# Kernel tuning notes

Measured on AMD Instinct MI355X. Metric: run time of the kernel, lower is better.

The kernel has to match this reference:

```python
import jax, jax.numpy as jnp
import numpy as np

N_NODES = 50000
N_EDGES = 800000
N_GRAPHS = 64
F_IN = 128
HID = 64
HEADS = 4
N_CLS = 10
NEG_SLOPE = 0.2


def _glorot(key, shape):
    fan_in, fan_out = shape[-1], shape[-2] if len(shape) > 1 else shape[-1]
    lim = jnp.sqrt(6.0 / (fan_in + fan_out))
    return jax.random.uniform(key, shape, jnp.float32, -lim, lim)


def setup_inputs() -> dict:
    key = jax.random.key(0)
    ks = jax.random.split(key, 20)
    x = jax.random.normal(ks[0], (N_NODES, F_IN), jnp.float32)
    edge_index = jax.random.randint(ks[1], (2, N_EDGES), 0, N_NODES, jnp.int32)
    batch = jnp.sort(jax.random.randint(ks[2], (N_NODES,), 0, N_GRAPHS, jnp.int32))
    HC = HID * HEADS
    return {
        "x": x, "edge_index": edge_index, "batch": batch,
        # node embedding Linear(F_IN -> HID)
        "W_emb": _glorot(ks[3], (HID, F_IN)), "b_emb": jnp.zeros((HID,), jnp.float32),
        # gat1: HID -> HID, heads=4, concat
        "W1": _glorot(ks[4], (HC, HID)),
        "a_src1": _glorot(ks[5], (HEADS, HID)), "a_dst1": _glorot(ks[6], (HEADS, HID)),
        "b1": jnp.zeros((HC,), jnp.float32),
        # gat2: HC -> HID, heads=4, concat
        "W2": _glorot(ks[7], (HC, HC)),
        "a_src2": _glorot(ks[8], (HEADS, HID)), "a_dst2": _glorot(ks[9], (HEADS, HID)),
        "b2": jnp.zeros((HC,), jnp.float32),
        # gat3: HC -> HID, heads=1, mean
        "W3": _glorot(ks[10], (HID, HC)),
        "a_src3": _glorot(ks[11], (1, HID)), "a_dst3": _glorot(ks[12], (1, HID)),
        "b3": jnp.zeros((HID,), jnp.float32),
        # classifier: Linear(2*HID -> HID), ReLU, Linear(HID -> N_CLS)
        "Wc1": _glorot(ks[13], (HID, 2 * HID)), "bc1": jnp.zeros((HID,), jnp.float32),
        "Wc2": _glorot(ks[14], (N_CLS, HID)), "bc2": jnp.zeros((N_CLS,), jnp.float32),
    }


def _gat_layer(x, src, dst, W, a_src, a_dst, b, concat):
    """PyG-style GATConv (eval mode, self-loops already in src/dst)."""
    N = x.shape[0]
    H, C = a_src.shape
    h = (x @ W.T).reshape(N, H, C)                       # [N,H,C]
    s = jnp.einsum("nhc,hc->nh", h, a_src)               # [N,H]
    d = jnp.einsum("nhc,hc->nh", h, a_dst)               # [N,H]
    e = jax.nn.leaky_relu(s[src] + d[dst], NEG_SLOPE)    # [E,H]
    emax = jax.lax.stop_gradient(jax.ops.segment_max(e, dst, num_segments=N))
    emax = jnp.where(jnp.isfinite(emax), emax, 0.0)
    ex = jnp.exp(e - emax[dst])
    den = jax.ops.segment_sum(ex, dst, num_segments=N)   # [N,H]
    alpha = ex / (den[dst] + 1e-16)                      # segment softmax
    out = jax.ops.segment_sum(h[src] * alpha[:, :, None], dst, num_segments=N)
    out = out.reshape(N, H * C) if concat else out.mean(axis=1)
    return out + b


def reference(x, edge_index, batch, W_emb, b_emb, W1, a_src1, a_dst1, b1,
              W2, a_src2, a_dst2, b2, W3, a_src3, a_dst3, b3, Wc1, bc1, Wc2, bc2):
    N = x.shape[0]
    loops = jnp.arange(N, dtype=edge_index.dtype)
    src = jnp.concatenate([edge_index[0], loops])
    dst = jnp.concatenate([edge_index[1], loops])

    h = x @ W_emb.T + b_emb
    h = jax.nn.elu(_gat_layer(h, src, dst, W1, a_src1, a_dst1, b1, True))
    h = jax.nn.elu(_gat_layer(h, src, dst, W2, a_src2, a_dst2, b2, True))
    h = jax.nn.elu(_gat_layer(h, src, dst, W3, a_src3, a_dst3, b3, False))

    counts = jax.ops.segment_sum(jnp.ones((N,), h.dtype), batch, num_segments=N_GRAPHS)
    mean = jax.ops.segment_sum(h, batch, num_segments=N_GRAPHS) / jnp.maximum(counts, 1.0)[:, None]
    mx = jax.ops.segment_max(h, batch, num_segments=N_GRAPHS)
    mx = jnp.where(counts[:, None] > 0, mx, 0.0)
    g = jnp.concatenate([mean, mx], axis=1)              # [B, 2*HID]

    g = jax.nn.relu(g @ Wc1.T + bc1)
    return g @ Wc2.T + bc2                               # [B, N_CLS]
```

## Files before the change

### kernel.cpp

```cpp
#include <hip/hip_runtime.h>
#include <math.h>

#define NG 64
#define F_IN 128
#define NEG_SLOPE 0.2f

typedef __attribute__((ext_vector_type(8))) short s16x8;
typedef __attribute__((ext_vector_type(4))) float f32x4;

static __device__ __forceinline__ float elu_f(float x) { return x > 0.f ? x : expm1f(x); }
static __device__ __forceinline__ float lrelu(float x) { return x > 0.f ? x : NEG_SLOPE * x; }
static __device__ __forceinline__ unsigned enc_f32(float x) {
    unsigned u = __float_as_uint(x);
    return (u & 0x80000000u) ? ~u : (u | 0x80000000u);
}
static __device__ __forceinline__ float dec_f32(unsigned u) {
    unsigned b = (u & 0x80000000u) ? (u & 0x7fffffffu) : ~u;
    return __uint_as_float(b);
}
static __device__ __forceinline__ unsigned short bf16_rn(float x) {
    unsigned u = __float_as_uint(x);
    unsigned r = u + 0x7FFFu + ((u >> 16) & 1u);
    return (unsigned short)(r >> 16);
}
static __device__ __forceinline__ float bf16_to_f32(unsigned short h) {
    return __uint_as_float(((unsigned)h) << 16);
}

static __device__ __forceinline__ size_t fragaddr(int row, int k, int K) {
    return ((size_t)(row >> 4) * (K >> 5) + (k >> 5)) * 512
         + (size_t)(((k & 31) >> 3) * 128 + (row & 15) * 8 + (k & 7));
}

__global__ void convert_frag(const float* __restrict__ in, unsigned short* __restrict__ hi,
                             unsigned short* __restrict__ lo, int R, int K) {
    int t = blockIdx.x * blockDim.x + threadIdx.x;
    if (t * 8 >= R * K) return;
    int row = (t * 8) / K;
    int k0 = (t * 8) % K;
    float4 v0 = *(const float4*)&in[(size_t)row * K + k0];
    float4 v1 = *(const float4*)&in[(size_t)row * K + k0 + 4];
    float v[8] = {v0.x, v0.y, v0.z, v0.w, v1.x, v1.y, v1.z, v1.w};
    unsigned short h[8], l[8];
    #pragma unroll
    for (int i = 0; i < 8; ++i) {
        h[i] = bf16_rn(v[i]);
        l[i] = bf16_rn(v[i] - bf16_to_f32(h[i]));
    }
    size_t a = fragaddr(row, k0, K);
    *(ushort4*)&hi[a]     = make_ushort4(h[0], h[1], h[2], h[3]);
    *(ushort4*)&hi[a + 4] = make_ushort4(h[4], h[5], h[6], h[7]);
    *(ushort4*)&lo[a]     = make_ushort4(l[0], l[1], l[2], l[3]);
    *(ushort4*)&lo[a + 4] = make_ushort4(l[4], l[5], l[6], l[7]);
}

__global__ void uvec_kernel(const float* __restrict__ W1, const float* __restrict__ a1s,
                            const float* __restrict__ a1d,
                            float* __restrict__ us, float* __restrict__ ud) {
    int h = threadIdx.x >> 6;
    int i = threadIdx.x & 63;
    float s = 0.f, d = 0.f;
    for (int o = 0; o < 64; ++o) {
        float w = W1[(h * 64 + o) * 64 + i];
        s = fmaf(w, a1s[h * 64 + o], s);
        d = fmaf(w, a1d[h * 64 + o], d);
    }
    us[h * 64 + i] = s;
    ud[h * 64 + i] = d;
}

__global__ void hist_kernel(const int* __restrict__ ei, int* __restrict__ cnt, int E, int N) {
    int e = blockIdx.x * blockDim.x + threadIdx.x;
    int ET = E + N;
    if (e >= ET) return;
    int dst = (e < E) ? ei[E + e] : (e - E);
    atomicAdd(&cnt[dst], 1);
}

__global__ void scan1_kernel(const int* __restrict__ cnt, int* __restrict__ excl,
                             int* __restrict__ bsum, int n) {
    __shared__ int sm[256];
    int t = threadIdx.x;
    int base = blockIdx.x * 1024 + t * 4;
    int v[4];
    #pragma unroll
    for (int u = 0; u < 4; ++u) { int idx = base + u; v[u] = (idx < n) ? cnt[idx] : 0; }
    int tsum = v[0] + v[1] + v[2] + v[3];
    sm[t] = tsum;
    __syncthreads();
    for (int off = 1; off < 256; off <<= 1) {
        int y = (t >= off) ? sm[t - off] : 0;
        __syncthreads();
        sm[t] += y;
        __syncthreads();
    }
    int run = sm[t] - tsum;
    #pragma unroll
    for (int u = 0; u < 4; ++u) {
        int idx = base + u;
        if (idx < n) excl[idx] = run;
        run += v[u];
    }
    if (t == 255) bsum[blockIdx.x] = sm[255];
}

__global__ void scan2_kernel(int* __restrict__ bsum, int* __restrict__ offs, int nb, int n) {
    if (blockIdx.x == 0 && threadIdx.x == 0) {
        int run = 0;
        for (int b = 0; b < nb; ++b) { int t = bsum[b]; bsum[b] = run; run += t; }
        offs[n] = run;
    }
}

__global__ void scan3_kernel(int* __restrict__ offs, const int* __restrict__ bsum, int n) {
    int base = blockIdx.x * 1024 + threadIdx.x * 4;
    int add = bsum[blockIdx.x];
    #pragma unroll
    for (int u = 0; u < 4; ++u) { int idx = base + u; if (idx < n) offs[idx] += add; }
}

__global__ void scatter_kernel(const int* __restrict__ ei, const int* __restrict__ offs,
                               int* __restrict__ cursor, int* __restrict__ csr_src, int E, int N) {
    int e = blockIdx.x * blockDim.x + threadIdx.x;
    int ET = E + N;
    if (e >= ET) return;
    int src, dst;
    if (e < E) { src = ei[e]; dst = ei[E + e]; }
    else       { src = e - E; dst = e - E; }
    int pos = offs[dst] + atomicAdd(&cursor[dst], 1);
    csr_src[pos] = src;
}

template<int K, int AK, int BN, int HATT, bool SHARED, bool SLICED, bool DO_ELU, int OUTM>
__global__ __launch_bounds__(256) void gemm_frag(const unsigned short* __restrict__ Ahi,
                                                 const unsigned short* __restrict__ Alo,
                                                 const unsigned short* __restrict__ Whi,
                                                 const unsigned short* __restrict__ Wlo,
                                                 void* __restrict__ OutV,
                                                 unsigned short* __restrict__ Ohi,
                                                 unsigned short* __restrict__ Olo,
                                                 int M,
                                                 const float* __restrict__ bias,
                                                 const float* __restrict__ asrc,
                                                 const float* __restrict__ adst,
                                                 float* __restrict__ S, float* __restrict__ D,
                                                 int N) {
    constexpr int RF = (BN == 256) ? 4 : 2;
    const int t = threadIdx.x;
    const int lane = t & 63;
    const int w = t >> 6;
    const int lj = lane & 15;
    const int kg = lane >> 4;
    const int n0 = blockIdx.x * ((BN == 256) ? 64 : 128);
    const int m0 = blockIdx.y * BN;
    const int rbase = (BN == 256) ? 0 : w * 32;
    const int cbase = (BN == 256) ? w * 64 : 0;
    const int aoff = SLICED ? blockIdx.y * K : 0;
    const unsigned short* __restrict__ WhiB = SLICED ? Whi + (size_t)blockIdx.y * BN * K : Whi;
    const unsigned short* __restrict__ WloB = SLICED ? Wlo + (size_t)blockIdx.y * BN * K : Wlo;

    f32x4 acc[RF][4];
    #pragma unroll
    for (int rf = 0; rf < RF; ++rf)
        #pragma unroll
        for (int cf = 0; cf < 4; ++cf) acc[rf][cf] = (f32x4){0.f, 0.f, 0.f, 0.f};

    for (int kc = 0; kc < K; kc += 32) {
        s16x8 ah[RF], al[RF];
        #pragma unroll
        for (int rf = 0; rf < RF; ++rf) {
            size_t a = fragaddr(n0 + rbase + rf * 16 + lj, aoff + kc + kg * 8, AK);
            ah[rf] = *(const s16x8*)&Ahi[a];
            al[rf] = *(const s16x8*)&Alo[a];
        }
        #pragma unroll
        for (int cf = 0; cf < 4; ++cf) {
            int bcol = (SLICED ? 0 : m0) + cbase + cf * 16 + lj;
            size_t b = fragaddr(bcol, kc + kg * 8, K);
            s16x8 bh = *(const s16x8*)&WhiB[b];
            s16x8 bl = *(const s16x8*)&WloB[b];
            #pragma unroll
            for (int rf = 0; rf < RF; ++rf) {
                acc[rf][cf] = __builtin_amdgcn_mfma_f32_16x16x32_bf16(ah[rf], bh, acc[rf][cf], 0, 0, 0);
                acc[rf][cf] = __builtin_amdgcn_mfma_f32_16x16x32_bf16(ah[rf], bl, acc[rf][cf], 0, 0, 0);
                acc[rf][cf] = __builtin_amdgcn_mfma_f32_16x16x32_bf16(al[rf], bh, acc[rf][cf], 0, 0, 0);
            }
        }
    }

    #pragma unroll
    for (int cf = 0; cf < 4; ++cf) {
        int gcol = m0 + cbase + cf * 16 + lj;
        float bv = bias ? bias[gcol] : 0.f;
        #pragma unroll
        for (int rf = 0; rf < RF; ++rf) {
            #pragma unroll
            for (int r = 0; r < 4; ++r) {
                int gn = n0 + rbase + rf * 16 + (lane >> 4) * 4 + r;
                if (gn < N) {
                    float o = acc[rf][cf][r] + bv;
                    if (DO_ELU) o = elu_f(o);
                    if (OUTM == 0) {
                        ((float*)OutV)[(size_t)gn * M + gcol] = o;
                    } else if (OUTM == 1) {
                        ((unsigned short*)OutV)[(size_t)gn * M + gcol] = bf16_rn(o);
                    } else {
                        unsigned short hv = bf16_rn(o);
                        unsigned short lv = bf16_rn(o - bf16_to_f32(hv));
                        size_t a2 = fragaddr(gn, gcol, M);
                        Ohi[a2] = hv; Olo[a2] = lv;
                    }
                }
            }
        }
    }
    if (HATT > 0) {
        const int HS = SHARED ? HATT : 1;
        #pragma unroll
        for (int hh = 0; hh < HS; ++hh) {
            const int head = SHARED ? hh : w;
            float aw[4], dw[4], bw[4];
            #pragma unroll
            for (int c2 = 0; c2 < 4; ++c2) {
                aw[c2] = asrc[head * 64 + c2 * 16 + lj];
                dw[c2] = adst[head * 64 + c2 * 16 + lj];
                bw[c2] = bias ? bias[m0 + cbase + c2 * 16 + lj] : 0.f;
            }
            #pragma unroll
            for (int rf = 0; rf < RF; ++rf) {
                #pragma unroll
                for (int r = 0; r < 4; ++r) {
                    float sp = 0.f, dp = 0.f;
                    #pragma unroll
                    for (int c2 = 0; c2 < 4; ++c2) {
                        float vv = acc[rf][c2][r] + bw[c2];
                        sp = fmaf(vv, aw[c2], sp);
                        dp = fmaf(vv, dw[c2], dp);
                    }
                    #pragma unroll
                    for (int off = 1; off < 16; off <<= 1) {
                        sp += __shfl_xor(sp, off);
                        dp += __shfl_xor(dp, off);
                    }
                    if (lj == 0) {
                        int gn = n0 + rbase + rf * 16 + (lane >> 4) * 4 + r;
                        if (gn < N) { S[gn * HATT + head] = sp; D[gn * HATT + head] = dp; }
                    }
                }
            }
        }
    }
}

__global__ __launch_bounds__(256, 8) void gat_agg_x(const float* __restrict__ xA,
                                                    const float* __restrict__ s,
                                                    const float* __restrict__ d,
                                                    const int* __restrict__ offs,
                                                    const int* __restrict__ csr_src,
                                                    unsigned short* __restrict__ Gh,
                                                    unsigned short* __restrict__ Gl,
                                                    int N) {
    __shared__ float stash[4][64 * 5];
    int wv = threadIdx.x >> 6;
    int lane = threadIdx.x & 63;
    int node = (blockIdx.x * blockDim.x + threadIdx.x) >> 6;
    if (node >= N) return;
    float* st = stash[wv];
    int e0 = offs[node], e1 = offs[node + 1];
    float4 dv4 = *(const float4*)&d[node * 4];
    float dd[4] = {dv4.x, dv4.y, dv4.z, dv4.w};
    float mrun[4] = {-INFINITY, -INFINITY, -INFINITY, -INFINITY};
    float den[4] = {0.f, 0.f, 0.f, 0.f};
    float acc[4] = {0.f, 0.f, 0.f, 0.f};

    for (int base = e0; base < e1; base += 64) {
        int cnt = min(64, e1 - base);
        float ev[4] = {-INFINITY, -INFINITY, -INFINITY, -INFINITY};
        if (lane < cnt) {
            int src = csr_src[base + lane];
            float4 sv = *(const float4*)&s[src * 4];
            ev[0] = lrelu(sv.x + dd[0]); ev[1] = lrelu(sv.y + dd[1]);
            ev[2] = lrelu(sv.z + dd[2]); ev[3] = lrelu(sv.w + dd[3]);
            st[lane * 5 + 0] = ev[0]; st[lane * 5 + 1] = ev[1];
            st[lane * 5 + 2] = ev[2]; st[lane * 5 + 3] = ev[3];
            st[lane * 5 + 4] = __int_as_float(src);
        }
        #pragma unroll
        for (int h = 0; h < 4; ++h) {
            float m = ev[h];
            #pragma unroll
            for (int off = 32; off; off >>= 1) m = fmaxf(m, __shfl_xor(m, off));
            float mnew = fmaxf(mrun[h], m);
            float scale = __expf(mrun[h] - mnew);
            acc[h] *= scale; den[h] *= scale;
            mrun[h] = mnew;
        }
        int k = 0;
        for (; k + 4 <= cnt; k += 4) {
            int si[4];
            #pragma unroll
            for (int u = 0; u < 4; ++u) si[u] = __float_as_int(st[(k + u) * 5 + 4]);
            float vx[4];
            #pragma unroll
            for (int u = 0; u < 4; ++u) vx[u] = xA[(size_t)si[u] * 64 + lane];
            #pragma unroll
            for (int u = 0; u < 4; ++u) {
                #pragma unroll
                for (int h = 0; h < 4; ++h) {
                    float p = __expf(st[(k + u) * 5 + h] - mrun[h]);
                    den[h] += p;
                    acc[h] = fmaf(p, vx[u], acc[h]);
                }
            }
        }
        for (; k < cnt; ++k) {
            int src = __float_as_int(st[k * 5 + 4]);
            float v = xA[(size_t)src * 64 + lane];
            #pragma unroll
            for (int h = 0; h < 4; ++h) {
                float p = __expf(st[k * 5 + h] - mrun[h]);
                den[h] += p;
                acc[h] = fmaf(p, v, acc[h]);
            }
        }
    }
    #pragma unroll
    for (int h = 0; h < 4; ++h) {
        float v = acc[h] / (den[h] + 1e-16f);
        unsigned short hv = bf16_rn(v);
        unsigned short lv = bf16_rn(v - bf16_to_f32(hv));
        size_t a = fragaddr(node, h * 64 + lane, 256);
        Gh[a] = hv; Gl[a] = lv;
    }
}

template<int H, bool FRAGOUT>
__global__ __launch_bounds__(256, 8) void gat_agg(const unsigned short* __restrict__ hp,
                                                  const float* __restrict__ s,
                                                  const float* __restrict__ d,
                                                  const int* __restrict__ offs,
                                                  const int* __restrict__ csr_src,
                                                  const float* __restrict__ bias,
                                                  float* __restrict__ outF,
                                                  unsigned short* __restrict__ outHi,
                                                  unsigned short* __restrict__ outLo,
                                                  int N) {
    const int SW = (H == 4) ? 5 : 2;
    __shared__ float stash[4][64 * 5];
    int wv = threadIdx.x >> 6;
    int lane = threadIdx.x & 63;
    int node = (blockIdx.x * blockDim.x + threadIdx.x) >> 6;
    if (node >= N) return;
    float* st = stash[wv];
    int e0 = offs[node], e1 = offs[node + 1];

    float dd[H];
    #pragma unroll
    for (int h = 0; h < H; ++h) dd[h] = d[node * H + h];

    const int hd = (H == 4) ? (lane >> 4) : 0;

    float mrun = -INFINITY;
    float acc0 = 0.f, acc1 = 0.f, acc2 = 0.f, acc3 = 0.f, den = 0.f;

    for (int base = e0; base < e1; base += 64) {
        int cnt = min(64, e1 - base);
        float ev[H];
        #pragma unroll
        for (int h = 0; h < H; ++h) ev[h] = -INFINITY;
        if (lane < cnt) {
            int src = csr_src[base + lane];
            if (H == 4) {
                float4 sv = *(const float4*)&s[src * 4];
                ev[0] = lrelu(sv.x + dd[0]); ev[1] = lrelu(sv.y + dd[1]);
                ev[2] = lrelu(sv.z + dd[2]); ev[3] = lrelu(sv.w + dd[3]);
                st[lane * 5 + 0] = ev[0]; st[lane * 5 + 1] = ev[1];
                st[lane * 5 + 2] = ev[2]; st[lane * 5 + 3] = ev[3];
                st[lane * 5 + 4] = __int_as_float(src);
            } else {
                ev[0] = lrelu(s[src] + dd[0]);
                st[lane * 2 + 0] = ev[0];
                st[lane * 2 + 1] = __int_as_float(src);
            }
        }
        float mc[H];
        #pragma unroll
        for (int h = 0; h < H; ++h) {
            float m = ev[h];
            #pragma unroll
            for (int off = 32; off; off >>= 1) m = fmaxf(m, __shfl_xor(m, off));
            mc[h] = m;
        }
        float mch = mc[0];
        if (H == 4)
            mch = (lane & 32) ? ((lane & 16) ? mc[3] : mc[2]) : ((lane & 16) ? mc[1] : mc[0]);
        float mnew = fmaxf(mrun, mch);
        float scale = __expf(mrun - mnew);
        acc0 *= scale; acc1 *= scale; acc2 *= scale; acc3 *= scale; den *= scale;
        mrun = mnew;

        int k = 0;
        for (; k + 4 <= cnt; k += 4) {
            float ea = st[(k + 0) * SW + hd];
            float eb = st[(k + 1) * SW + hd];
            float ec = st[(k + 2) * SW + hd];
            float ed = st[(k + 3) * SW + hd];
            int sa = __float_as_int(st[(k + 0) * SW + SW - 1]);
            int sb = __float_as_int(st[(k + 1) * SW + SW - 1]);
            int sc = __float_as_int(st[(k + 2) * SW + SW - 1]);
            int sd_ = __float_as_int(st[(k + 3) * SW + SW - 1]);
            float pa = __expf(ea - mrun);
            float pb = __expf(eb - mrun);
            float pc = __expf(ec - mrun);
            float pd = __expf(ed - mrun);
            den += (pa + pb) + (pc + pd);
            if (H == 4) {
                uint2 ua = *(const uint2*)&hp[(size_t)sa * 256 + lane * 4];
                uint2 ub = *(const uint2*)&hp[(size_t)sb * 256 + lane * 4];
                uint2 uc = *(const uint2*)&hp[(size_t)sc * 256 + lane * 4];
                uint2 ud = *(const uint2*)&hp[(size_t)sd_ * 256 + lane * 4];
                acc0 = fmaf(pa, __uint_as_float((ua.x & 0xffffu) << 16), acc0);
                acc1 = fmaf(pa, __uint_as_float(ua.x & 0xffff0000u), acc1);
                acc2 = fmaf(pa, __uint_as_float((ua.y & 0xffffu) << 16), acc2);
                acc3 = fmaf(pa, __uint_as_float(ua.y & 0xffff0000u), acc3);
                acc0 = fmaf(pb, __uint_as_float((ub.x & 0xffffu) << 16), acc0);
                acc1 = fmaf(pb, __uint_as_float(ub.x & 0xffff0000u), acc1);
                acc2 = fmaf(pb, __uint_as_float((ub.y & 0xffffu) << 16), acc2);
                acc3 = fmaf(pb, __uint_as_float(ub.y & 0xffff0000u), acc3);
                acc0 = fmaf(pc, __uint_as_float((uc.x & 0xffffu) << 16), acc0);
                acc1 = fmaf(pc, __uint_as_float(uc.x & 0xffff0000u), acc1);
                acc2 = fmaf(pc, __uint_as_float((uc.y & 0xffffu) << 16), acc2);
                acc3 = fmaf(pc, __uint_as_float(uc.y & 0xffff0000u), acc3);
                acc0 = fmaf(pd, __uint_as_float((ud.x & 0xffffu) << 16), acc0);
                acc1 = fmaf(pd, __uint_as_float(ud.x & 0xffff0000u), acc1);
                acc2 = fmaf(pd, __uint_as_float((ud.y & 0xffffu) << 16), acc2);
                acc3 = fmaf(pd, __uint_as_float(ud.y & 0xffff0000u), acc3);
            } else {
                float ha = bf16_to_f32(hp[(size_t)sa * 64 + lane]);
                float hb = bf16_to_f32(hp[(size_t)sb * 64 + lane]);
                float hc = bf16_to_f32(hp[(size_t)sc * 64 + lane]);
                float hdv = bf16_to_f32(hp[(size_t)sd_ * 64 + lane]);
                acc0 = fmaf(pa, ha, acc0);
                acc0 = fmaf(pb, hb, acc0);
                acc0 = fmaf(pc, hc, acc0);
                acc0 = fmaf(pd, hdv, acc0);
            }
        }
        for (; k < cnt; ++k) {
            float e = st[k * SW + hd];
            int src = __float_as_int(st[k * SW + SW - 1]);
            float p = __expf(e - mrun);
            den += p;
            if (H == 4) {
                uint2 uv = *(const uint2*)&hp[(size_t)src * 256 + lane * 4];
                acc0 = fmaf(p, __uint_as_float((uv.x & 0xffffu) << 16), acc0);
                acc1 = fmaf(p, __uint_as_float(uv.x & 0xffff0000u), acc1);
                acc2 = fmaf(p, __uint_as_float((uv.y & 0xffffu) << 16), acc2);
                acc3 = fmaf(p, __uint_as_float(uv.y & 0xffff0000u), acc3);
            } else {
                acc0 = fmaf(p, bf16_to_f32(hp[(size_t)src * 64 + lane]), acc0);
            }
        }
    }

    float inv = 1.0f / (den + 1e-16f);
    if (H == 4) {
        float4 bv = *(const float4*)&bias[lane * 4];
        float o0 = elu_f(acc0 * inv + bv.x);
        float o1 = elu_f(acc1 * inv + bv.y);
        float o2 = elu_f(acc2 * inv + bv.z);
        float o3 = elu_f(acc3 * inv + bv.w);
        if (FRAGOUT) {
            unsigned short h0 = bf16_rn(o0), h1 = bf16_rn(o1), h2 = bf16_rn(o2), h3 = bf16_rn(o3);
            ushort4 hq = make_ushort4(h0, h1, h2, h3);
            ushort4 lq = make_ushort4(bf16_rn(o0 - bf16_to_f32(h0)),
                                      bf16_rn(o1 - bf16_to_f32(h1)),
                                      bf16_rn(o2 - bf16_to_f32(h2)),
                                      bf16_rn(o3 - bf16_to_f32(h3)));
            size_t a = fragaddr(node, lane * 4, 256);
            *(ushort4*)&outHi[a] = hq;
            *(ushort4*)&outLo[a] = lq;
        } else {
            float4 o = make_float4(o0, o1, o2, o3);
            *(float4*)&outF[(size_t)node * 256 + lane * 4] = o;
        }
    } else {
        outF[(size_t)node * 64 + lane] = elu_f(acc0 * inv + bias[lane]);
    }
}

__global__ void pool_init(float* gsum, unsigned* gmax, int* gcnt) {
    int t = blockIdx.x * blockDim.x + threadIdx.x;
    if (t < NG * 64) { gsum[t] = 0.f; gmax[t] = enc_f32(-INFINITY); }
    if (t < NG) gcnt[t] = 0;
}

__global__ void pool_reduce(const float* __restrict__ h3, const int* __restrict__ batch,
                            float* __restrict__ gsum, unsigned* __restrict__ gmax,
                            int* __restrict__ gcnt, int N, int per) {
    int w = (blockIdx.x * blockDim.x + threadIdx.x) >> 6;
    int lane = threadIdx.x & 63;
    int n0 = w * per;
    int n1 = min(N, n0 + per);
    float lsum = 0.f, lmax = -INFINITY;
    int cur = -1, cnt = 0;
    for (int n = n0; n < n1; ++n) {
        int g = batch[n];
        if (g != cur) {
            if (cur >= 0) {
                atomicAdd(&gsum[cur * 64 + lane], lsum);
                atomicMax(&gmax[cur * 64 + lane], enc_f32(lmax));
                if (lane == 0) atomicAdd(&gcnt[cur], cnt);
            }
            cur = g; lsum = 0.f; lmax = -INFINITY; cnt = 0;
        }
        float v = h3[(size_t)n * 64 + lane];
        lsum += v; lmax = fmaxf(lmax, v); cnt++;
    }
    if (cur >= 0) {
        atomicAdd(&gsum[cur * 64 + lane], lsum);
        atomicMax(&gmax[cur * 64 + lane], enc_f32(lmax));
        if (lane == 0) atomicAdd(&gcnt[cur], cnt);
    }
}

__global__ __launch_bounds__(128) void classifier(const float* __restrict__ gsum,
                                                  const unsigned* __restrict__ gmax,
                                                  const int* __restrict__ gcnt,
                                                  const float* __restrict__ Wc1,
                                                  const float* __restrict__ bc1,
                                                  const float* __restrict__ Wc2,
                                                  const float* __restrict__ bc2,
                                                  float* __restrict__ out) {
    __shared__ float gv[128];
    __shared__ float z1[64];
    int g = blockIdx.x, t = threadIdx.x;
    int cnt = gcnt[g];
    if (t < 64) {
        gv[t] = gsum[g * 64 + t] / fmaxf((float)cnt, 1.f);
    } else {
        float mx = dec_f32(gmax[g * 64 + (t - 64)]);
        gv[t] = (cnt > 0) ? mx : 0.f;
    }
    __syncthreads();
    if (t < 64) {
        float a = bc1[t];
        for (int k = 0; k < 128; ++k) a = fmaf(Wc1[t * 128 + k], gv[k], a);
        z1[t] = a > 0.f ? a : 0.f;
    }
    __syncthreads();
    if (t < 10) {
        float a = bc2[t];
        for (int k = 0; k < 64; ++k) a = fmaf(Wc2[t * 64 + k], z1[k], a);
        out[g * 10 + t] = a;
    }
}

extern "C" void kernel_launch(void* const* d_in, const int* in_sizes, int n_in,
                              void* d_out, int out_size, void* d_ws, size_t ws_size,
                              hipStream_t stream) {
    const float* x      = (const float*)d_in[0];
    const int*   ei     = (const int*)d_in[1];
    const int*   batch  = (const int*)d_in[2];
    const float* W_emb  = (const float*)d_in[3];
    const float* b_emb  = (const float*)d_in[4];
    const float* W1     = (const float*)d_in[5];
    const float* as1    = (const float*)d_in[6];
    const float* ad1    = (const float*)d_in[7];
    const float* b1     = (const float*)d_in[8];
    const float* W2     = (const float*)d_in[9];
    const float* as2    = (const float*)d_in[10];
    const float* ad2    = (const float*)d_in[11];
    const float* b2     = (const float*)d_in[12];
    const float* W3     = (const float*)d_in[13];
    const float* as3    = (const float*)d_in[14];
    const float* ad3    = (const float*)d_in[15];
    const float* b3     = (const float*)d_in[16];
    const float* Wc1    = (const float*)d_in[17];
    const float* bc1    = (const float*)d_in[18];
    const float* Wc2    = (const float*)d_in[19];
    const float* bc2    = (const float*)d_in[20];

    const int N = in_sizes[0] / F_IN;
    const int E = in_sizes[1] / 2;
    const int ET = E + N;
    const int GB64 = (N + 63) / 64;
    const int GB128 = (N + 127) / 128;
    const int ROWS_FR = ((N + 255) / 256) * 256;
    const size_t FR128 = (size_t)(ROWS_FR / 16) * (128 / 32) * 512;
    const size_t FR256 = (size_t)(ROWS_FR / 16) * (256 / 32) * 512;

    size_t off = 0;
    auto alloc = [&](size_t bytes) -> void* {
        void* p = (char*)d_ws + off;
        off += (bytes + 255) & ~(size_t)255;
        return p;
    };
    unsigned short* Xh  = (unsigned short*)alloc(FR128 * 2);
    unsigned short* Xl  = (unsigned short*)alloc(FR128 * 2);
    float*          Aemb= (float*)alloc((size_t)N * 64 * 4);
    unsigned short* Gh  = (unsigned short*)alloc(FR256 * 2);
    unsigned short* Gl  = (unsigned short*)alloc(FR256 * 2);
    unsigned short* C1h = (unsigned short*)alloc(FR256 * 2);
    unsigned short* C1l = (unsigned short*)alloc(FR256 * 2);
    unsigned short* H2b = (unsigned short*)alloc((size_t)N * 256 * 2);
    unsigned short* WhE = (unsigned short*)alloc(64 * 128 * 2);
    unsigned short* WlE = (unsigned short*)alloc(64 * 128 * 2);
    unsigned short* Wh1 = (unsigned short*)alloc(256 * 64 * 2);
    unsigned short* Wl1 = (unsigned short*)alloc(256 * 64 * 2);
    unsigned short* Wh2 = (unsigned short*)alloc(256 * 256 * 2);
    unsigned short* Wl2 = (unsigned short*)alloc(256 * 256 * 2);
    unsigned short* Wh3 = (unsigned short*)alloc(64 * 256 * 2);
    unsigned short* Wl3 = (unsigned short*)alloc(64 * 256 * 2);
    float*    us1     = (float*)alloc(4 * 64 * 4);
    float*    ud1     = (float*)alloc(4 * 64 * 4);
    float*    S       = (float*)alloc((size_t)N * 4 * 4);
    float*    D       = (float*)alloc((size_t)N * 4 * 4);
    int*      offs    = (int*)alloc((size_t)(N + 1) * 4);
    int*      cnt     = (int*)alloc((size_t)N * 4);
    int*      bsum    = (int*)alloc(64 * 4);
    int*      csr_src = (int*)alloc((size_t)ET * 4);
    float*    gsum    = (float*)alloc(NG * 64 * 4);
    unsigned* gmax    = (unsigned*)alloc(NG * 64 * 4);
    int*      gcnt    = (int*)alloc(NG * 4);
    (void)ws_size; (void)n_in; (void)out_size;

    const int SCB = (N + 1023) / 1024;

    convert_frag<<<(N * 128 / 8 + 255) / 256, 256, 0, stream>>>(x, Xh, Xl, N, 128);
    convert_frag<<<4, 256, 0, stream>>>(W_emb, WhE, WlE, 64, 128);
    convert_frag<<<8, 256, 0, stream>>>(W1, Wh1, Wl1, 256, 64);
    convert_frag<<<32, 256, 0, stream>>>(W2, Wh2, Wl2, 256, 256);
    convert_frag<<<8, 256, 0, stream>>>(W3, Wh3, Wl3, 64, 256);
    uvec_kernel<<<1, 256, 0, stream>>>(W1, as1, ad1, us1, ud1);

    hipMemsetAsync(cnt, 0, (size_t)N * 4, stream);
    hist_kernel<<<(ET + 255) / 256, 256, 0, stream>>>(ei, cnt, E, N);
    scan1_kernel<<<SCB, 256, 0, stream>>>(cnt, offs, bsum, N);
    scan2_kernel<<<1, 64, 0, stream>>>(bsum, offs, SCB, N);
    scan3_kernel<<<SCB, 256, 0, stream>>>(offs, bsum, N);
    hipMemsetAsync(cnt, 0, (size_t)N * 4, stream);
    scatter_kernel<<<(ET + 255) / 256, 256, 0, stream>>>(ei, offs, cnt, csr_src, E, N);

    const int NWV = (N * 64 + 255) / 256;

    gemm_frag<128, 128, 64, 4, true, false, false, 0><<<dim3(GB128, 1), 256, 0, stream>>>(
        Xh, Xl, WhE, WlE, Aemb, nullptr, nullptr, 64, b_emb, us1, ud1, S, D, N);
    gat_agg_x<<<NWV, 256, 0, stream>>>(Aemb, S, D, offs, csr_src, Gh, Gl, N);
    gemm_frag<64, 256, 64, 0, false, true, true, 3><<<dim3(GB128, 4), 256, 0, stream>>>(
        Gh, Gl, Wh1, Wl1, nullptr, C1h, C1l, 256, b1, nullptr, nullptr, nullptr, nullptr, N);
    gemm_frag<256, 256, 256, 4, false, false, false, 1><<<dim3(GB64, 1), 256, 0, stream>>>(
        C1h, C1l, Wh2, Wl2, H2b, nullptr, nullptr, 256, nullptr, as2, ad2, S, D, N);
    gat_agg<4, true><<<NWV, 256, 0, stream>>>(H2b, S, D, offs, csr_src, b2,
                                              nullptr, Gh, Gl, N);
    gemm_frag<256, 256, 64, 1, true, false, false, 1><<<dim3(GB128, 1), 256, 0, stream>>>(
        Gh, Gl, Wh3, Wl3, (unsigned short*)Aemb, nullptr, nullptr, 64, nullptr, as3, ad3, S, D, N);
    gat_agg<1, false><<<NWV, 256, 0, stream>>>((const unsigned short*)Aemb, S, D, offs, csr_src,
                                               b3, (float*)H2b, nullptr, nullptr, N);

    pool_init<<<16, 256, 0, stream>>>(gsum, gmax, gcnt);
    const int PBLK = 512;
    int per = (N + PBLK * 4 - 1) / (PBLK * 4);
    pool_reduce<<<PBLK, 256, 0, stream>>>((const float*)H2b, batch, gsum, gmax, gcnt, N, per);
    classifier<<<NG, 128, 0, stream>>>(gsum, gmax, gcnt, Wc1, bc1, Wc2, bc2, (float*)d_out);
}
```

Baseline: 539.1 us.

## Store embedding as bf16, split layer-2 aggregation across two waves, fuse setup kernels

The embedding GEMM now writes bf16 instead of fp32, which halves the gather traffic in the first attention aggregation. The 4-head aggregation is split so each node gets two wavefronts, each covering two heads. This doubles parallelism and shortens the per-node serial edge loop, at the cost of reading the edge list twice. The four weight-conversion launches become one kernel, and the scatter cursor is initialised from the scan, which removes a memset and an offset load. The bf16 embedding adds rounding error to layer-1 inputs.

```diff
diff --git a/kernel.cpp b/kernel.cpp
--- a/kernel.cpp
+++ b/kernel.cpp
@@ -30,6 +30,21 @@
 static __device__ __forceinline__ size_t fragaddr(int row, int k, int K) {
     return ((size_t)(row >> 4) * (K >> 5) + (k >> 5)) * 512
          + (size_t)(((k & 31) >> 3) * 128 + (row & 15) * 8 + (k & 7));
+}
+
+static __device__ __forceinline__ void frag_store8(const float* v, unsigned short* hi,
+                                                   unsigned short* lo, int row, int k0, int K) {
+    unsigned short h[8], l[8];
+    #pragma unroll
+    for (int i = 0; i < 8; ++i) {
+        h[i] = bf16_rn(v[i]);
+        l[i] = bf16_rn(v[i] - bf16_to_f32(h[i]));
+    }
+    size_t a = fragaddr(row, k0, K);
+    *(ushort4*)&hi[a]     = make_ushort4(h[0], h[1], h[2], h[3]);
+    *(ushort4*)&hi[a + 4] = make_ushort4(h[4], h[5], h[6], h[7]);
+    *(ushort4*)&lo[a]     = make_ushort4(l[0], l[1], l[2], l[3]);
+    *(ushort4*)&lo[a + 4] = make_ushort4(l[4], l[5], l[6], l[7]);
 }
 
 __global__ void convert_frag(const float* __restrict__ in, unsigned short* __restrict__ hi,
@@ -41,17 +56,29 @@
     float4 v0 = *(const float4*)&in[(size_t)row * K + k0];
     float4 v1 = *(const float4*)&in[(size_t)row * K + k0 + 4];
     float v[8] = {v0.x, v0.y, v0.z, v0.w, v1.x, v1.y, v1.z, v1.w};
-    unsigned short h[8], l[8];
-    #pragma unroll
-    for (int i = 0; i < 8; ++i) {
-        h[i] = bf16_rn(v[i]);
-        l[i] = bf16_rn(v[i] - bf16_to_f32(h[i]));
-    }
-    size_t a = fragaddr(row, k0, K);
-    *(ushort4*)&hi[a]     = make_ushort4(h[0], h[1], h[2], h[3]);
-    *(ushort4*)&hi[a + 4] = make_ushort4(h[4], h[5], h[6], h[7]);
-    *(ushort4*)&lo[a]     = make_ushort4(l[0], l[1], l[2], l[3]);
-    *(ushort4*)&lo[a + 4] = make_ushort4(l[4], l[5], l[6], l[7]);
+    frag_store8(v, hi, lo, row, k0, K);
+}
+
+__global__ void convert_weights(const float* __restrict__ We, const float* __restrict__ W1,
+                                const float* __restrict__ W2, const float* __restrict__ W3,
+                                unsigned short* WhE, unsigned short* WlE,
+                                unsigned short* Wh1, unsigned short* Wl1,
+                                unsigned short* Wh2, unsigned short* Wl2,
+                                unsigned short* Wh3, unsigned short* Wl3) {
+    int b = blockIdx.x;
+    const float* in; unsigned short* hi; unsigned short* lo; int R, K, base;
+    if (b < 4)       { in = We; hi = WhE; lo = WlE; R = 64;  K = 128; base = 0; }
+    else if (b < 12) { in = W1; hi = Wh1; lo = Wl1; R = 256; K = 64;  base = 4; }
+    else if (b < 44) { in = W2; hi = Wh2; lo = Wl2; R = 256; K = 256; base = 12; }
+    else             { in = W3; hi = Wh3; lo = Wl3; R = 64;  K = 256; base = 44; }
+    int t = (b - base) * 256 + threadIdx.x;
+    if (t * 8 >= R * K) return;
+    int row = (t * 8) / K;
+    int k0 = (t * 8) % K;
+    float4 v0 = *(const float4*)&in[(size_t)row * K + k0];
+    float4 v1 = *(const float4*)&in[(size_t)row * K + k0 + 4];
+    float v[8] = {v0.x, v0.y, v0.z, v0.w, v1.x, v1.y, v1.z, v1.w};
+    frag_store8(v, hi, lo, row, k0, K);
 }
 
 __global__ void uvec_kernel(const float* __restrict__ W1, const float* __restrict__ a1s,
@@ -112,22 +139,26 @@
     }
 }
 
-__global__ void scan3_kernel(int* __restrict__ offs, const int* __restrict__ bsum, int n) {
+__global__ void scan3_kernel(int* __restrict__ offs, const int* __restrict__ bsum,
+                             int* __restrict__ cur, int n) {
     int base = blockIdx.x * 1024 + threadIdx.x * 4;
     int add = bsum[blockIdx.x];
     #pragma unroll
-    for (int u = 0; u < 4; ++u) { int idx = base + u; if (idx < n) offs[idx] += add; }
-}
-
-__global__ void scatter_kernel(const int* __restrict__ ei, const int* __restrict__ offs,
-                               int* __restrict__ cursor, int* __restrict__ csr_src, int E, int N) {
+    for (int u = 0; u < 4; ++u) {
+        int idx = base + u;
+        if (idx < n) { int v = offs[idx] + add; offs[idx] = v; cur[idx] = v; }
+    }
+}
+
+__global__ void scatter_kernel(const int* __restrict__ ei, int* __restrict__ cur,
+                               int* __restrict__ csr_src, int E, int N) {
     int e = blockIdx.x * blockDim.x + threadIdx.x;
     int ET = E + N;
     if (e >= ET) return;
     int src, dst;
     if (e < E) { src = ei[e]; dst = ei[E + e]; }
     else       { src = e - E; dst = e - E; }
-    int pos = offs[dst] + atomicAdd(&cursor[dst], 1);
+    int pos = atomicAdd(&cur[dst], 1);
     csr_src[pos] = src;
 }
 
@@ -252,7 +283,7 @@
     }
 }
 
-__global__ __launch_bounds__(256, 8) void gat_agg_x(const float* __restrict__ xA,
+__global__ __launch_bounds__(256, 8) void gat_agg_x(const unsigned short* __restrict__ xb,
                                                     const float* __restrict__ s,
                                                     const float* __restrict__ d,
                                                     const int* __restrict__ offs,
@@ -302,7 +333,7 @@
             for (int u = 0; u < 4; ++u) si[u] = __float_as_int(st[(k + u) * 5 + 4]);
             float vx[4];
             #pragma unroll
-            for (int u = 0; u < 4; ++u) vx[u] = xA[(size_t)si[u] * 64 + lane];
+            for (int u = 0; u < 4; ++u) vx[u] = bf16_to_f32(xb[(size_t)si[u] * 64 + lane]);
             #pragma unroll
             for (int u = 0; u < 4; ++u) {
                 #pragma unroll
@@ -315,7 +346,7 @@
         }
         for (; k < cnt; ++k) {
             int src = __float_as_int(st[k * 5 + 4]);
-            float v = xA[(size_t)src * 64 + lane];
+            float v = bf16_to_f32(xb[(size_t)src * 64 + lane]);
             #pragma unroll
             for (int h = 0; h < 4; ++h) {
                 float p = __expf(st[k * 5 + h] - mrun[h]);
@@ -334,159 +365,185 @@
     }
 }
 
-template<int H, bool FRAGOUT>
-__global__ __launch_bounds__(256, 8) void gat_agg(const unsigned short* __restrict__ hp,
-                                                  const float* __restrict__ s,
-                                                  const float* __restrict__ d,
-                                                  const int* __restrict__ offs,
-                                                  const int* __restrict__ csr_src,
-                                                  const float* __restrict__ bias,
-                                                  float* __restrict__ outF,
-                                                  unsigned short* __restrict__ outHi,
-                                                  unsigned short* __restrict__ outLo,
-                                                  int N) {
-    const int SW = (H == 4) ? 5 : 2;
-    __shared__ float stash[4][64 * 5];
+template<bool FRAGOUT>
+__global__ __launch_bounds__(256, 8) void gat_agg2(const unsigned short* __restrict__ hp,
+                                                   const float* __restrict__ s,
+                                                   const float* __restrict__ d,
+                                                   const int* __restrict__ offs,
+                                                   const int* __restrict__ csr_src,
+                                                   const float* __restrict__ bias,
+                                                   float* __restrict__ outF,
+                                                   unsigned short* __restrict__ outHi,
+                                                   unsigned short* __restrict__ outLo,
+                                                   int N) {
+    __shared__ float stash[4][64 * 3];
+    int wv = threadIdx.x >> 6;
+    int lane = threadIdx.x & 63;
+    int gw = (blockIdx.x * blockDim.x + threadIdx.x) >> 6;
+    int node = gw >> 1;
+    int half = gw & 1;
+    if (node >= N) return;
+    float* st = stash[wv];
+    int e0 = offs[node], e1 = offs[node + 1];
+    const int h0 = half * 2;
+    float2 dv = *(const float2*)&d[node * 4 + h0];
+    const float dd0 = dv.x, dd1 = dv.y;
+    const int hh = lane >> 5;
+    const int ci = (lane & 31) * 2;
+    const int rowoff = (h0 + hh) * 64 + ci;
+
+    float mrun = -INFINITY;
+    float a0 = 0.f, a1 = 0.f, den = 0.f;
+
+    for (int base = e0; base < e1; base += 64) {
+        int cnt = min(64, e1 - base);
+        float ev0 = -INFINITY, ev1 = -INFINITY;
+        if (lane < cnt) {
+            int src = csr_src[base + lane];
+            float2 sv = *(const float2*)&s[src * 4 + h0];
+            ev0 = lrelu(sv.x + dd0);
+            ev1 = lrelu(sv.y + dd1);
+            st[lane * 3 + 0] = ev0;
+            st[lane * 3 + 1] = ev1;
+            st[lane * 3 + 2] = __int_as_float(src);
+        }
+        float m0 = ev0, m1 = ev1;
+        #pragma unroll
+        for (int off = 32; off; off >>= 1) {
+            m0 = fmaxf(m0, __shfl_xor(m0, off));
+            m1 = fmaxf(m1, __shfl_xor(m1, off));
+        }
+        float mch = hh ? m1 : m0;
+        float mnew = fmaxf(mrun, mch);
+        float scale = __expf(mrun - mnew);
+        a0 *= scale; a1 *= scale; den *= scale;
+        mrun = mnew;
+
+        int k = 0;
+        for (; k + 4 <= cnt; k += 4) {
+            float ea = st[(k + 0) * 3 + hh];
+            float eb = st[(k + 1) * 3 + hh];
+            float ec = st[(k + 2) * 3 + hh];
+            float ed = st[(k + 3) * 3 + hh];
+            int sa = __float_as_int(st[(k + 0) * 3 + 2]);
+            int sb = __float_as_int(st[(k + 1) * 3 + 2]);
+            int sc = __float_as_int(st[(k + 2) * 3 + 2]);
+            int sd_ = __float_as_int(st[(k + 3) * 3 + 2]);
+            float pa = __expf(ea - mrun);
+            float pb = __expf(eb - mrun);
+            float pc = __expf(ec - mrun);
+            float pd = __expf(ed - mrun);
+            den += (pa + pb) + (pc + pd);
+            unsigned ua = *(const unsigned*)&hp[(size_t)sa * 256 + rowoff];
+            unsigned ub = *(const unsigned*)&hp[(size_t)sb * 256 + rowoff];
+            unsigned uc = *(const unsigned*)&hp[(size_t)sc * 256 + rowoff];
+            unsigned ud = *(const unsigned*)&hp[(size_t)sd_ * 256 + rowoff];
+            a0 = fmaf(pa, __uint_as_float((ua & 0xffffu) << 16), a0);
+            a1 = fmaf(pa, __uint_as_float(ua & 0xffff0000u), a1);
+            a0 = fmaf(pb, __uint_as_float((ub & 0xffffu) << 16), a0);
+            a1 = fmaf(pb, __uint_as_float(ub & 0xffff0000u), a1);
+            a0 = fmaf(pc, __uint_as_float((uc & 0xffffu) << 16), a0);
+            a1 = fmaf(pc, __uint_as_float(uc & 0xffff0000u), a1);
+            a0 = fmaf(pd, __uint_as_float((ud & 0xffffu) << 16), a0);
+            a1 = fmaf(pd, __uint_as_float(ud & 0xffff0000u), a1);
+        }
+        for (; k < cnt; ++k) {
+            float e = st[k * 3 + hh];
+            int src = __float_as_int(st[k * 3 + 2]);
+            float p = __expf(e - mrun);
+            den += p;
+            unsigned uv = *(const unsigned*)&hp[(size_t)src * 256 + rowoff];
+            a0 = fmaf(p, __uint_as_float((uv & 0xffffu) << 16), a0);
+            a1 = fmaf(p, __uint_as_float(uv & 0xffff0000u), a1);
+        }
+    }
+
+    float inv = 1.0f / (den + 1e-16f);
+    float2 bv = *(const float2*)&bias[rowoff];
+    float o0 = elu_f(a0 * inv + bv.x);
+    float o1 = elu_f(a1 * inv + bv.y);
+    if (FRAGOUT) {
+        unsigned short hv0 = bf16_rn(o0), hv1 = bf16_rn(o1);
+        unsigned short lv0 = bf16_rn(o0 - bf16_to_f32(hv0));
+        unsigned short lv1 = bf16_rn(o1 - bf16_to_f32(hv1));
+        size_t a = fragaddr(node, rowoff, 256);
+        *(ushort2*)&outHi[a] = make_ushort2(hv0, hv1);
+        *(ushort2*)&outLo[a] = make_ushort2(lv0, lv1);
+    } else {
+        *(float2*)&outF[(size_t)node * 256 + rowoff] = make_float2(o0, o1);
+    }
+}
+
+__global__ __launch_bounds__(256, 8) void gat_agg1(const unsigned short* __restrict__ hp,
+                                                   const float* __restrict__ s,
+                                                   const float* __restrict__ d,
+                                                   const int* __restrict__ offs,
+                                                   const int* __restrict__ csr_src,
+                                                   const float* __restrict__ bias,
+                                                   float* __restrict__ outF, int N) {
+    __shared__ float stash[4][64 * 2];
     int wv = threadIdx.x >> 6;
     int lane = threadIdx.x & 63;
     int node = (blockIdx.x * blockDim.x + threadIdx.x) >> 6;
     if (node >= N) return;
     float* st = stash[wv];
     int e0 = offs[node], e1 = offs[node + 1];
-
-    float dd[H];
-    #pragma unroll
-    for (int h = 0; h < H; ++h) dd[h] = d[node * H + h];
-
-    const int hd = (H == 4) ? (lane >> 4) : 0;
+    float dd = d[node];
 
     float mrun = -INFINITY;
-    float acc0 = 0.f, acc1 = 0.f, acc2 = 0.f, acc3 = 0.f, den = 0.f;
+    float acc0 = 0.f, den = 0.f;
 
     for (int base = e0; base < e1; base += 64) {
         int cnt = min(64, e1 - base);
-        float ev[H];
-        #pragma unroll
-        for (int h = 0; h < H; ++h) ev[h] = -INFINITY;
+        float ev = -INFINITY;
         if (lane < cnt) {
             int src = csr_src[base + lane];
-            if (H == 4) {
-                float4 sv = *(const float4*)&s[src * 4];
-                ev[0] = lrelu(sv.x + dd[0]); ev[1] = lrelu(sv.y + dd[1]);
-                ev[2] = lrelu(sv.z + dd[2]); ev[3] = lrelu(sv.w + dd[3]);
-                st[lane * 5 + 0] = ev[0]; st[lane * 5 + 1] = ev[1];
-                st[lane * 5 + 2] = ev[2]; st[lane * 5 + 3] = ev[3];
-                st[lane * 5 + 4] = __int_as_float(src);
-            } else {
-                ev[0] = lrelu(s[src] + dd[0]);
-                st[lane * 2 + 0] = ev[0];
-                st[lane * 2 + 1] = __int_as_float(src);
-            }
-        }
-        float mc[H];
+            ev = lrelu(s[src] + dd);
+            st[lane * 2 + 0] = ev;
+            st[lane * 2 + 1] = __int_as_float(src);
+        }
+        float m = ev;
         #pragma unroll
-        for (int h = 0; h < H; ++h) {
-            float m = ev[h];
-            #pragma unroll
-            for (int off = 32; off; off >>= 1) m = fmaxf(m, __shfl_xor(m, off));
-            mc[h] = m;
-        }
-        float mch = mc[0];
-        if (H == 4)
-            mch = (lane & 32) ? ((lane & 16) ? mc[3] : mc[2]) : ((lane & 16) ? mc[1] : mc[0]);
-        float mnew = fmaxf(mrun, mch);
+        for (int off = 32; off; off >>= 1) m = fmaxf(m, __shfl_xor(m, off));
+        float mnew = fmaxf(mrun, m);
         float scale = __expf(mrun - mnew);
-        acc0 *= scale; acc1 *= scale; acc2 *= scale; acc3 *= scale; den *= scale;
+        acc0 *= scale; den *= scale;
         mrun = mnew;
 
         int k = 0;
         for (; k + 4 <= cnt; k += 4) {
-            float ea = st[(k + 0) * SW + hd];
-            float eb = st[(k + 1) * SW + hd];
-            float ec = st[(k + 2) * SW + hd];
-            float ed = st[(k + 3) * SW + hd];
-            int sa = __float_as_int(st[(k + 0) * SW + SW - 1]);
-            int sb = __float_as_int(st[(k + 1) * SW + SW - 1]);
-            int sc = __float_as_int(st[(k + 2) * SW + SW - 1]);
-            int sd_ = __float_as_int(st[(k + 3) * SW + SW - 1]);
+            float ea = st[(k + 0) * 2];
+            float eb = st[(k + 1) * 2];
+            float ec = st[(k + 2) * 2];
+            float ed = st[(k + 3) * 2];
+            int sa = __float_as_int(st[(k + 0) * 2 + 1]);
+            int sb = __float_as_int(st[(k + 1) * 2 + 1]);
+            int sc = __float_as_int(st[(k + 2) * 2 + 1]);
+            int sd_ = __float_as_int(st[(k + 3) * 2 + 1]);
             float pa = __expf(ea - mrun);
             float pb = __expf(eb - mrun);
             float pc = __expf(ec - mrun);
             float pd = __expf(ed - mrun);
             den += (pa + pb) + (pc + pd);
-            if (H == 4) {
-                uint2 ua = *(const uint2*)&hp[(size_t)sa * 256 + lane * 4];
-                uint2 ub = *(const uint2*)&hp[(size_t)sb * 256 + lane * 4];
-                uint2 uc = *(const uint2*)&hp[(size_t)sc * 256 + lane * 4];
-                uint2 ud = *(const uint2*)&hp[(size_t)sd_ * 256 + lane * 4];
-                acc0 = fmaf(pa, __uint_as_float((ua.x & 0xffffu) << 16), acc0);
-                acc1 = fmaf(pa, __uint_as_float(ua.x & 0xffff0000u), acc1);
-                acc2 = fmaf(pa, __uint_as_float((ua.y & 0xffffu) << 16), acc2);
-                acc3 = fmaf(pa, __uint_as_float(ua.y & 0xffff0000u), acc3);
-                acc0 = fmaf(pb, __uint_as_float((ub.x & 0xffffu) << 16), acc0);
-                acc1 = fmaf(pb, __uint_as_float(ub.x & 0xffff0000u), acc1);
-                acc2 = fmaf(pb, __uint_as_float((ub.y & 0xffffu) << 16), acc2);
-                acc3 = fmaf(pb, __uint_as_float(ub.y & 0xffff0000u), acc3);
-                acc0 = fmaf(pc, __uint_as_float((uc.x & 0xffffu) << 16), acc0);
-                acc1 = fmaf(pc, __uint_as_float(uc.x & 0xffff0000u), acc1);
-                acc2 = fmaf(pc, __uint_as_float((uc.y & 0xffffu) << 16), acc2);
-                acc3 = fmaf(pc, __uint_as_float(uc.y & 0xffff0000u), acc3);
-                acc0 = fmaf(pd, __uint_as_float((ud.x & 0xffffu) << 16), acc0);
-                acc1 = fmaf(pd, __uint_as_float(ud.x & 0xffff0000u), acc1);
-                acc2 = fmaf(pd, __uint_as_float((ud.y & 0xffffu) << 16), acc2);
-                acc3 = fmaf(pd, __uint_as_float(ud.y & 0xffff0000u), acc3);
-            } else {
-                float ha = bf16_to_f32(hp[(size_t)sa * 64 + lane]);
-                float hb = bf16_to_f32(hp[(size_t)sb * 64 + lane]);
-                float hc = bf16_to_f32(hp[(size_t)sc * 64 + lane]);
-                float hdv = bf16_to_f32(hp[(size_t)sd_ * 64 + lane]);
-                acc0 = fmaf(pa, ha, acc0);
-                acc0 = fmaf(pb, hb, acc0);
-                acc0 = fmaf(pc, hc, acc0);
-                acc0 = fmaf(pd, hdv, acc0);
-            }
+            float ha = bf16_to_f32(hp[(size_t)sa * 64 + lane]);
+            float hb = bf16_to_f32(hp[(size_t)sb * 64 + lane]);
+            float hc = bf16_to_f32(hp[(size_t)sc * 64 + lane]);
+            float hdv = bf16_to_f32(hp[(size_t)sd_ * 64 + lane]);
+            acc0 = fmaf(pa, ha, acc0);
+            acc0 = fmaf(pb, hb, acc0);
+            acc0 = fmaf(pc, hc, acc0);
+            acc0 = fmaf(pd, hdv, acc0);
         }
         for (; k < cnt; ++k) {
-            float e = st[k * SW + hd];
-            int src = __float_as_int(st[k * SW + SW - 1]);
+            float e = st[k * 2];
+            int src = __float_as_int(st[k * 2 + 1]);
             float p = __expf(e - mrun);
             den += p;
-            if (H == 4) {
-                uint2 uv = *(const uint2*)&hp[(size_t)src * 256 + lane * 4];
-                acc0 = fmaf(p, __uint_as_float((uv.x & 0xffffu) << 16), acc0);
-                acc1 = fmaf(p, __uint_as_float(uv.x & 0xffff0000u), acc1);
-                acc2 = fmaf(p, __uint_as_float((uv.y & 0xffffu) << 16), acc2);
-                acc3 = fmaf(p, __uint_as_float(uv.y & 0xffff0000u), acc3);
-            } else {
-                acc0 = fmaf(p, bf16_to_f32(hp[(size_t)src * 64 + lane]), acc0);
-            }
-        }
-    }
-
+            acc0 = fmaf(p, bf16_to_f32(hp[(size_t)src * 64 + lane]), acc0);
+        }
+    }
     float inv = 1.0f / (den + 1e-16f);
-    if (H == 4) {
-        float4 bv = *(const float4*)&bias[lane * 4];
-        float o0 = elu_f(acc0 * inv + bv.x);
-        float o1 = elu_f(acc1 * inv + bv.y);
-        float o2 = elu_f(acc2 * inv + bv.z);
-        float o3 = elu_f(acc3 * inv + bv.w);
-        if (FRAGOUT) {
-            unsigned short h0 = bf16_rn(o0), h1 = bf16_rn(o1), h2 = bf16_rn(o2), h3 = bf16_rn(o3);
-            ushort4 hq = make_ushort4(h0, h1, h2, h3);
-            ushort4 lq = make_ushort4(bf16_rn(o0 - bf16_to_f32(h0)),
-                                      bf16_rn(o1 - bf16_to_f32(h1)),
-                                      bf16_rn(o2 - bf16_to_f32(h2)),
-                                      bf16_rn(o3 - bf16_to_f32(h3)));
-            size_t a = fragaddr(node, lane * 4, 256);
-            *(ushort4*)&outHi[a] = hq;
-            *(ushort4*)&outLo[a] = lq;
-        } else {
-            float4 o = make_float4(o0, o1, o2, o3);
-            *(float4*)&outF[(size_t)node * 256 + lane * 4] = o;
-        }
-    } else {
-        outF[(size_t)node * 64 + lane] = elu_f(acc0 * inv + bias[lane]);
-    }
+    outF[(size_t)node * 64 + lane] = elu_f(acc0 * inv + bias[lane]);
 }
 
 __global__ void pool_init(float* gsum, unsigned* gmax, int* gcnt) {
@@ -598,7 +655,7 @@
     };
     unsigned short* Xh  = (unsigned short*)alloc(FR128 * 2);
     unsigned short* Xl  = (unsigned short*)alloc(FR128 * 2);
-    float*          Aemb= (float*)alloc((size_t)N * 64 * 4);
+    unsigned short* Aemb= (unsigned short*)alloc((size_t)N * 64 * 2);
     unsigned short* Gh  = (unsigned short*)alloc(FR256 * 2);
     unsigned short* Gl  = (unsigned short*)alloc(FR256 * 2);
     unsigned short* C1h = (unsigned short*)alloc(FR256 * 2);
@@ -628,35 +685,32 @@
     const int SCB = (N + 1023) / 1024;
 
     convert_frag<<<(N * 128 / 8 + 255) / 256, 256, 0, stream>>>(x, Xh, Xl, N, 128);
-    convert_frag<<<4, 256, 0, stream>>>(W_emb, WhE, WlE, 64, 128);
-    convert_frag<<<8, 256, 0, stream>>>(W1, Wh1, Wl1, 256, 64);
-    convert_frag<<<32, 256, 0, stream>>>(W2, Wh2, Wl2, 256, 256);
-    convert_frag<<<8, 256, 0, stream>>>(W3, Wh3, Wl3, 64, 256);
+    convert_weights<<<52, 256, 0, stream>>>(W_emb, W1, W2, W3, WhE, WlE, Wh1, Wl1,
+                                            Wh2, Wl2, Wh3, Wl3);
     uvec_kernel<<<1, 256, 0, stream>>>(W1, as1, ad1, us1, ud1);
 
     hipMemsetAsync(cnt, 0, (size_t)N * 4, stream);
     hist_kernel<<<(ET + 255) / 256, 256, 0, stream>>>(ei, cnt, E, N);
     scan1_kernel<<<SCB, 256, 0, stream>>>(cnt, offs, bsum, N);
     scan2_kernel<<<1, 64, 0, stream>>>(bsum, offs, SCB, N);
-    scan3_kernel<<<SCB, 256, 0, stream>>>(offs, bsum, N);
-    hipMemsetAsync(cnt, 0, (size_t)N * 4, stream);
-    scatter_kernel<<<(ET + 255) / 256, 256, 0, stream>>>(ei, offs, cnt, csr_src, E, N);
+    scan3_kernel<<<SCB, 256, 0, stream>>>(offs, bsum, cnt, N);
+    scatter_kernel<<<(ET + 255) / 256, 256, 0, stream>>>(ei, cnt, csr_src, E, N);
 
     const int NWV = (N * 64 + 255) / 256;
-
-    gemm_frag<128, 128, 64, 4, true, false, false, 0><<<dim3(GB128, 1), 256, 0, stream>>>(
+    const int NWV2 = (N * 128 + 255) / 256;
+
+    gemm_frag<128, 128, 64, 4, true, false, false, 1><<<dim3(GB128, 1), 256, 0, stream>>>(
         Xh, Xl, WhE, WlE, Aemb, nullptr, nullptr, 64, b_emb, us1, ud1, S, D, N);
     gat_agg_x<<<NWV, 256, 0, stream>>>(Aemb, S, D, offs, csr_src, Gh, Gl, N);
     gemm_frag<64, 256, 64, 0, false, true, true, 3><<<dim3(GB128, 4), 256, 0, stream>>>(
         Gh, Gl, Wh1, Wl1, nullptr, C1h, C1l, 256, b1, nullptr, nullptr, nullptr, nullptr, N);
     gemm_frag<256, 256, 256, 4, false, false, false, 1><<<dim3(GB64, 1), 256, 0, stream>>>(
         C1h, C1l, Wh2, Wl2, H2b, nullptr, nullptr, 256, nullptr, as2, ad2, S, D, N);
-    gat_agg<4, true><<<NWV, 256, 0, stream>>>(H2b, S, D, offs, csr_src, b2,
-                                              nullptr, Gh, Gl, N);
+    gat_agg2<true><<<NWV2, 256, 0, stream>>>(H2b, S, D, offs, csr_src, b2,
+                                             nullptr, Gh, Gl, N);
     gemm_frag<256, 256, 64, 1, true, false, false, 1><<<dim3(GB128, 1), 256, 0, stream>>>(
-        Gh, Gl, Wh3, Wl3, (unsigned short*)Aemb, nullptr, nullptr, 64, nullptr, as3, ad3, S, D, N);
-    gat_agg<1, false><<<NWV, 256, 0, stream>>>((const unsigned short*)Aemb, S, D, offs, csr_src,
-                                               b3, (float*)H2b, nullptr, nullptr, N);
+        Gh, Gl, Wh3, Wl3, Aemb, nullptr, nullptr, 64, nullptr, as3, ad3, S, D, N);
+    gat_agg1<<<NWV, 256, 0, stream>>>(Aemb, S, D, offs, csr_src, b3, (float*)H2b, N);
 
     pool_init<<<16, 256, 0, stream>>>(gsum, gmax, gcnt);
     const int PBLK = 512;
```

After: 543.7 us. About the same (+0.9%).
